# Kernel tuning notes

Measured on AMD Instinct MI355X. Metric: run time of the kernel, lower is better.

The kernel has to match this reference:

```python
import jax, jax.numpy as jnp
import numpy as np
from jax import lax

BOOST_STRENGTH = 0.5
WEIGHT_DENSITY = 0.05


def setup_inputs() -> dict:
    key = jax.random.key(0)
    k1, k2, k3, k4, k5 = jax.random.split(key, 5)
    batch, d_in, d_out = 16384, 512, 4096
    x = jax.random.normal(k1, (batch, d_in), dtype=jnp.float32)
    W = jax.random.normal(k2, (d_out, d_in), dtype=jnp.float32) * 0.05
    b = jax.random.normal(k3, (d_out,), dtype=jnp.float32) * 0.01
    w_mask = (jax.random.uniform(k4, (d_out, d_in)) < WEIGHT_DENSITY).astype(jnp.float32)
    # duty cycle buffer in [0, 0.1]
    duty_cycle = jax.random.uniform(k5, (d_out,), dtype=jnp.float32) * 0.1
    k = 205  # round(0.05 * 4096)
    return {"x": x, "W": W, "b": b, "w_mask": w_mask,
            "duty_cycle": duty_cycle, "k": k}


def reference(x, W, b, w_mask, duty_cycle, k):
    # SparseWeights: masked dense linear
    y = x @ (W * w_mask).T + b                      # [B, n]
    n = y.shape[-1]
    target_density = k / n
    # KWinners boosting: exp of duty-cycle deficit
    boost = jnp.exp(BOOST_STRENGTH * (target_density - duty_cycle))  # [n]
    boosted = y * boost                              # [B, n]
    # top-k threshold per row on boosted values
    thresh = lax.top_k(boosted, k)[0][..., -1:]      # [B, 1]
    # mask: keep ORIGINAL activations at winner positions
    return jnp.where(boosted >= thresh, y, 0.0)
```

## Files before the change

### kernel.cpp

```cpp
#include <hip/hip_runtime.h>
#include <stdint.h>
#include <math.h>


#define BATCH 16384
#define K_DIM 512
#define N_DIM 4096
#define RPB 4
#define MAXE 64

typedef float f32x4 __attribute__((ext_vector_type(4)));
typedef unsigned int u32;

__global__ void boost_kernel(const float* __restrict__ duty,
                             const int* __restrict__ kptr,
                             float* __restrict__ boost) {
  const int j = blockIdx.x * blockDim.x + threadIdx.x;
  if (j < N_DIM) {
    const float td = (float)((double)kptr[0] / (double)N_DIM);
    const float arg = 0.5f * (td - duty[j]);
    boost[j] = (float)exp((double)arg);
  }
}

__global__ __launch_bounds__(256) void compress_kernel(
    const float* __restrict__ W, const float* __restrict__ mask,
    unsigned short* __restrict__ cIdx, float* __restrict__ cVal,
    int* __restrict__ cnt) {
  const int j = blockIdx.x * 4 + (threadIdx.x >> 6);
  const int lane = threadIdx.x & 63;
  if (j >= N_DIM) return;
  const float* mr = mask + (size_t)j * K_DIM;
  const float* wr = W + (size_t)j * K_DIM;
  int base = 0;
#pragma unroll
  for (int c = 0; c < K_DIM / 64; ++c) {
    const int k = c * 64 + lane;
    const bool act = (mr[k] != 0.0f);
    const unsigned long long bal = __ballot(act);
    const int pos = __popcll(bal & ((1ull << lane) - 1ull));
    if (act && base + pos < MAXE) {
      cIdx[(size_t)j * MAXE + base + pos] = (unsigned short)k;
      cVal[(size_t)j * MAXE + base + pos] = wr[k];
    }
    base += (int)__popcll(bal);
  }
  if (lane == 0) cnt[j] = base < MAXE ? base : MAXE;
}

__global__ __launch_bounds__(256) void sort_kernel(
    const int* __restrict__ cnt, int* __restrict__ perm, int* __restrict__ tE) {
  __shared__ int hist[MAXE + 1];
  __shared__ int off[MAXE + 1];
  const int tid = threadIdx.x;
  if (tid <= MAXE) hist[tid] = 0;
  __syncthreads();
  for (int j = tid; j < N_DIM; j += 256) atomicAdd(&hist[cnt[j]], 1);
  __syncthreads();
  if (tid == 0) {
    int s = 0;
    for (int c = 0; c <= MAXE; ++c) { off[c] = s; s += hist[c]; }
  }
  __syncthreads();
  for (int j = tid; j < N_DIM; j += 256) {
    const int p = atomicAdd(&off[cnt[j]], 1);
    perm[p] = j;
  }
  __syncthreads();
  tE[tid] = cnt[perm[tid * 16 + 15]];
}

__global__ __launch_bounds__(256) void fill_kernel(
    const unsigned short* __restrict__ cIdx, const float* __restrict__ cVal,
    const int* __restrict__ cnt, const int* __restrict__ perm,
    uint2* __restrict__ pairT, int* __restrict__ orig) {
  const int s = blockIdx.x * 256 + threadIdx.x;
  const int j = perm[s];
  const int c = cnt[j];
  const int slot = (s & 15) * 256 + (s >> 4);
  orig[slot] = j;
#pragma unroll 4
  for (int e = 0; e < MAXE; ++e) {
    uint2 pr;
    if (e < c) {
      pr.x = (u32)cIdx[(size_t)j * MAXE + e] * 16u;
      pr.y = __float_as_uint(cVal[(size_t)j * MAXE + e]);
    } else {
      pr.x = 0u; pr.y = 0u;
    }
    pairT[(size_t)e * N_DIM + slot] = pr;
  }
}

__global__ __launch_bounds__(256) void fused_kernel(
    const float* __restrict__ x, const float* __restrict__ bvec,
    const uint2* __restrict__ pairT, const float* __restrict__ boost,
    const int* __restrict__ orig, const int* __restrict__ tE,
    const int* __restrict__ kptr, float* __restrict__ out) {
  __shared__ __align__(16) float smem[N_DIM];
  __shared__ u32 hist[256];
  __shared__ u32 s_prefix, s_kk;

  const int tid = threadIdx.x;
  const int row0 = blockIdx.x * RPB;

  for (int i = tid; i < K_DIM; i += 256)
#pragma unroll
    for (int r = 0; r < RPB; ++r)
      smem[i * 4 + r] = x[(size_t)(row0 + r) * K_DIM + i];

  const int myE = tE[tid];
  const int kk0 = kptr[0];
  float a[RPB][16];
#pragma unroll
  for (int r = 0; r < RPB; ++r)
#pragma unroll
    for (int u = 0; u < 16; ++u) a[r][u] = 0.0f;
  __syncthreads();

  for (int e = 0; e < myE; ++e) {
    const uint2* pe = pairT + (size_t)e * N_DIM + tid;
#pragma unroll
    for (int u = 0; u < 16; ++u) {
      const uint2 pr = pe[u * 256];
      const f32x4 xs = *(const f32x4*)((const char*)smem + pr.x);
      const float w = __uint_as_float(pr.y);
      a[0][u] = fmaf(w, xs[0], a[0][u]);
      a[1][u] = fmaf(w, xs[1], a[1][u]);
      a[2][u] = fmaf(w, xs[2], a[2][u]);
      a[3][u] = fmaf(w, xs[3], a[3][u]);
    }
  }

#pragma unroll 1
  for (int r = 0; r < RPB; ++r) {
    __syncthreads();
#pragma unroll
    for (int u = 0; u < 16; ++u)
      smem[orig[u * 256 + tid]] = a[r][u];
    if (tid == 0) { s_prefix = 0u; s_kk = (u32)kk0; }
    __syncthreads();

    float y[16], bl[16];
    u32 key[16];
#pragma unroll
    for (int u = 0; u < 16; ++u) {
      const int j = u * 256 + tid;
      y[u] = smem[j] + bvec[j];
      bl[u] = boost[j];
      const float t = y[u] * bl[u];
      const u32 v = __float_as_uint(t);
      key[u] = (v & 0x80000000u) ? ~v : (v | 0x80000000u);
    }

#pragma unroll 1
    for (int round = 0; round < 4; ++round) {
      const int shift = 24 - 8 * round;
      const u32 prefix = s_prefix;
      const u32 kk = s_kk;
      const u32 himask = round ? (0xFFFFFFFFu << (32 - 8 * round)) : 0u;
      hist[tid] = 0u;
      __syncthreads();
#pragma unroll
      for (int u = 0; u < 16; ++u)
        if ((key[u] & himask) == prefix)
          atomicAdd(&hist[(key[u] >> shift) & 255u], 1u);
      __syncthreads();
      if (tid < 64) {
        const int l = tid;
        const u32 h0 = hist[l * 4], h1 = hist[l * 4 + 1];
        const u32 h2 = hist[l * 4 + 2], h3 = hist[l * 4 + 3];
        const u32 s3 = h3, s2 = h2 + s3, s1 = h1 + s2, s0 = h0 + s1;
        u32 t = s0;
#pragma unroll
        for (int off = 1; off < 64; off <<= 1) {
          const u32 v = __shfl_down(t, off, 64);
          if (l + off < 64) t += v;
        }
        const u32 Eab = t - s0;
        const u32 S[5] = {Eab + s0, Eab + s1, Eab + s2, Eab + s3, Eab};
#pragma unroll
        for (int i = 0; i < 4; ++i)
          if (S[i] >= kk && S[i + 1] < kk) {
            s_prefix = prefix | ((u32)(l * 4 + i) << shift);
            s_kk = kk - S[i + 1];
          }
      }
      __syncthreads();
    }
    const u32 tkey = s_prefix;

    float* orow = out + (size_t)(row0 + r) * N_DIM;
#pragma unroll
    for (int u = 0; u < 16; ++u)
      orow[u * 256 + tid] = (key[u] >= tkey) ? y[u] : 0.0f;
  }
}

extern "C" void kernel_launch(void* const* d_in, const int* in_sizes, int n_in,
                              void* d_out, int out_size, void* d_ws, size_t ws_size,
                              hipStream_t stream) {
  const float* x     = (const float*)d_in[0];
  const float* W     = (const float*)d_in[1];
  const float* bvec  = (const float*)d_in[2];
  const float* wmask = (const float*)d_in[3];
  const float* duty  = (const float*)d_in[4];
  const int* kptr    = (const int*)d_in[5];
  float* out = (float*)d_out;

  uint8_t* ws = (uint8_t*)d_ws;
  unsigned short* cIdx = (unsigned short*)(ws);
  float* cVal          = (float*)(ws + (1u << 20));
  int* cnt             = (int*)(ws + (2u << 20));
  float* boost         = (float*)(ws + (2u << 20) + (64u << 10));
  int* perm            = (int*)(ws + (2u << 20) + (128u << 10));
  int* tE              = (int*)(ws + (2u << 20) + (192u << 10));
  int* orig            = (int*)(ws + (2u << 20) + (256u << 10));
  uint2* pairT         = (uint2*)(ws + (4u << 20));

  boost_kernel<<<16, 256, 0, stream>>>(duty, kptr, boost);
  compress_kernel<<<N_DIM / 4, 256, 0, stream>>>(W, wmask, cIdx, cVal, cnt);
  sort_kernel<<<1, 256, 0, stream>>>(cnt, perm, tE);
  fill_kernel<<<N_DIM / 256, 256, 0, stream>>>(cIdx, cVal, cnt, perm, pairT, orig);
  fused_kernel<<<BATCH / RPB, 256, 0, stream>>>(x, bvec, pairT, boost, orig, tE,
                                                kptr, out);
}
```

Before: 786.5 us.

## Batch radix-select across rows, double-buffer pair loads, raise occupancy hint

The sparse-accumulate loop now double-buffers its index/weight pair loads in registers, so the global loads for the next nonzero overlap with the FMAs on the current one. The per-row radix select is restructured so all four rows are processed together: each wavefront scans one row's histogram in parallel. This cuts the barrier count from about four rounds per row to four rounds in total. Bias and boost are now applied in the permuted domain before the select, and the masked output is scattered through shared memory for coalesced stores. The launch bound of four blocks per CU, together with the extra 32 pair registers, may force register spills.

```diff
diff --git a/kernel.cpp b/kernel.cpp
--- a/kernel.cpp
+++ b/kernel.cpp
@@ -92,14 +92,14 @@
   }
 }
 
-__global__ __launch_bounds__(256) void fused_kernel(
+__global__ __launch_bounds__(256, 4) void fused_kernel(
     const float* __restrict__ x, const float* __restrict__ bvec,
     const uint2* __restrict__ pairT, const float* __restrict__ boost,
     const int* __restrict__ orig, const int* __restrict__ tE,
     const int* __restrict__ kptr, float* __restrict__ out) {
   __shared__ __align__(16) float smem[N_DIM];
-  __shared__ u32 hist[256];
-  __shared__ u32 s_prefix, s_kk;
+  __shared__ u32 hist[4 * 256];
+  __shared__ u32 s_prefix[4], s_kk[4];
 
   const int tid = threadIdx.x;
   const int row0 = blockIdx.x * RPB;
@@ -118,82 +118,127 @@
     for (int u = 0; u < 16; ++u) a[r][u] = 0.0f;
   __syncthreads();
 
-  for (int e = 0; e < myE; ++e) {
-    const uint2* pe = pairT + (size_t)e * N_DIM + tid;
-#pragma unroll
-    for (int u = 0; u < 16; ++u) {
-      const uint2 pr = pe[u * 256];
-      const f32x4 xs = *(const f32x4*)((const char*)smem + pr.x);
-      const float w = __uint_as_float(pr.y);
+  uint2 prA[16], prB[16];
+  {
+    const uint2* p0 = pairT + tid;
+#pragma unroll
+    for (int u = 0; u < 16; ++u) prA[u] = p0[u * 256];
+  }
+  int e = 0;
+  for (; e + 2 <= myE; e += 2) {
+    const uint2* p1 = pairT + (size_t)(e + 1) * N_DIM + tid;
+#pragma unroll
+    for (int u = 0; u < 16; ++u) prB[u] = p1[u * 256];
+#pragma unroll
+    for (int u = 0; u < 16; ++u) {
+      const f32x4 xs = *(const f32x4*)((const char*)smem + prA[u].x);
+      const float w = __uint_as_float(prA[u].y);
       a[0][u] = fmaf(w, xs[0], a[0][u]);
       a[1][u] = fmaf(w, xs[1], a[1][u]);
       a[2][u] = fmaf(w, xs[2], a[2][u]);
       a[3][u] = fmaf(w, xs[3], a[3][u]);
     }
+    const uint2* p2 = pairT + (size_t)(e + 2) * N_DIM + tid;
+#pragma unroll
+    for (int u = 0; u < 16; ++u) prA[u] = p2[u * 256];
+#pragma unroll
+    for (int u = 0; u < 16; ++u) {
+      const f32x4 xs = *(const f32x4*)((const char*)smem + prB[u].x);
+      const float w = __uint_as_float(prB[u].y);
+      a[0][u] = fmaf(w, xs[0], a[0][u]);
+      a[1][u] = fmaf(w, xs[1], a[1][u]);
+      a[2][u] = fmaf(w, xs[2], a[2][u]);
+      a[3][u] = fmaf(w, xs[3], a[3][u]);
+    }
+  }
+  if (e < myE) {
+#pragma unroll
+    for (int u = 0; u < 16; ++u) {
+      const f32x4 xs = *(const f32x4*)((const char*)smem + prA[u].x);
+      const float w = __uint_as_float(prA[u].y);
+      a[0][u] = fmaf(w, xs[0], a[0][u]);
+      a[1][u] = fmaf(w, xs[1], a[1][u]);
+      a[2][u] = fmaf(w, xs[2], a[2][u]);
+      a[3][u] = fmaf(w, xs[3], a[3][u]);
+    }
+  }
+
+  int origId[16];
+  float bl[16];
+#pragma unroll
+  for (int u = 0; u < 16; ++u) origId[u] = orig[u * 256 + tid];
+#pragma unroll
+  for (int u = 0; u < 16; ++u) {
+    const float bj = bvec[origId[u]];
+    bl[u] = boost[origId[u]];
+#pragma unroll
+    for (int r = 0; r < RPB; ++r) a[r][u] += bj;
+  }
+
+  if (tid < 4) { s_prefix[tid] = 0u; s_kk[tid] = (u32)kk0; }
+
+#pragma unroll 1
+  for (int round = 0; round < 4; ++round) {
+    const int shift = 24 - 8 * round;
+    const u32 himask = round ? (0xFFFFFFFFu << (32 - 8 * round)) : 0u;
+#pragma unroll
+    for (int q = 0; q < 4; ++q) hist[q * 256 + tid] = 0u;
+    __syncthreads();
+#pragma unroll
+    for (int r = 0; r < RPB; ++r) {
+      const u32 prefix = s_prefix[r];
+#pragma unroll
+      for (int u = 0; u < 16; ++u) {
+        const float t = a[r][u] * bl[u];
+        const u32 v = __float_as_uint(t);
+        const u32 key = (v & 0x80000000u) ? ~v : (v | 0x80000000u);
+        if ((key & himask) == prefix)
+          atomicAdd(&hist[r * 256 + ((key >> shift) & 255u)], 1u);
+      }
+    }
+    __syncthreads();
+    {
+      const int w = tid >> 6;
+      const int l = tid & 63;
+      const u32 kk = s_kk[w];
+      const u32 prefix = s_prefix[w];
+      const u32 h0 = hist[w * 256 + l * 4],     h1 = hist[w * 256 + l * 4 + 1];
+      const u32 h2 = hist[w * 256 + l * 4 + 2], h3 = hist[w * 256 + l * 4 + 3];
+      const u32 s3 = h3, s2 = h2 + s3, s1 = h1 + s2, s0 = h0 + s1;
+      u32 t = s0;
+#pragma unroll
+      for (int off = 1; off < 64; off <<= 1) {
+        const u32 v = __shfl_down(t, off, 64);
+        if (l + off < 64) t += v;
+      }
+      const u32 Eab = t - s0;
+      const u32 S[5] = {Eab + s0, Eab + s1, Eab + s2, Eab + s3, Eab};
+#pragma unroll
+      for (int i = 0; i < 4; ++i)
+        if (S[i] >= kk && S[i + 1] < kk) {
+          s_prefix[w] = prefix | ((u32)(l * 4 + i) << shift);
+          s_kk[w] = kk - S[i + 1];
+        }
+    }
+    __syncthreads();
   }
 
 #pragma unroll 1
   for (int r = 0; r < RPB; ++r) {
-    __syncthreads();
+    const u32 tkey = s_prefix[r];
+    __syncthreads();
+#pragma unroll
+    for (int u = 0; u < 16; ++u) {
+      const float t = a[r][u] * bl[u];
+      const u32 v = __float_as_uint(t);
+      const u32 key = (v & 0x80000000u) ? ~v : (v | 0x80000000u);
+      smem[origId[u]] = (key >= tkey) ? a[r][u] : 0.0f;
+    }
+    __syncthreads();
+    float* orow = out + (size_t)(row0 + r) * N_DIM;
 #pragma unroll
     for (int u = 0; u < 16; ++u)
-      smem[orig[u * 256 + tid]] = a[r][u];
-    if (tid == 0) { s_prefix = 0u; s_kk = (u32)kk0; }
-    __syncthreads();
-
-    float y[16], bl[16];
-    u32 key[16];
-#pragma unroll
-    for (int u = 0; u < 16; ++u) {
-      const int j = u * 256 + tid;
-      y[u] = smem[j] + bvec[j];
-      bl[u] = boost[j];
-      const float t = y[u] * bl[u];
-      const u32 v = __float_as_uint(t);
-      key[u] = (v & 0x80000000u) ? ~v : (v | 0x80000000u);
-    }
-
-#pragma unroll 1
-    for (int round = 0; round < 4; ++round) {
-      const int shift = 24 - 8 * round;
-      const u32 prefix = s_prefix;
-      const u32 kk = s_kk;
-      const u32 himask = round ? (0xFFFFFFFFu << (32 - 8 * round)) : 0u;
-      hist[tid] = 0u;
-      __syncthreads();
-#pragma unroll
-      for (int u = 0; u < 16; ++u)
-        if ((key[u] & himask) == prefix)
-          atomicAdd(&hist[(key[u] >> shift) & 255u], 1u);
-      __syncthreads();
-      if (tid < 64) {
-        const int l = tid;
-        const u32 h0 = hist[l * 4], h1 = hist[l * 4 + 1];
-        const u32 h2 = hist[l * 4 + 2], h3 = hist[l * 4 + 3];
-        const u32 s3 = h3, s2 = h2 + s3, s1 = h1 + s2, s0 = h0 + s1;
-        u32 t = s0;
-#pragma unroll
-        for (int off = 1; off < 64; off <<= 1) {
-          const u32 v = __shfl_down(t, off, 64);
-          if (l + off < 64) t += v;
-        }
-        const u32 Eab = t - s0;
-        const u32 S[5] = {Eab + s0, Eab + s1, Eab + s2, Eab + s3, Eab};
-#pragma unroll
-        for (int i = 0; i < 4; ++i)
-          if (S[i] >= kk && S[i + 1] < kk) {
-            s_prefix = prefix | ((u32)(l * 4 + i) << shift);
-            s_kk = kk - S[i + 1];
-          }
-      }
-      __syncthreads();
-    }
-    const u32 tkey = s_prefix;
-
-    float* orow = out + (size_t)(row0 + r) * N_DIM;
-#pragma unroll
-    for (int u = 0; u < 16; ++u)
-      orow[u * 256 + tid] = (key[u] >= tkey) ? y[u] : 0.0f;
+      orow[u * 256 + tid] = smem[u * 256 + tid];
   }
 }
 
```

Result: slower. 1.297 ms (+64.8%).

## Radix-select on fixed-point keys in permuted order, add tie-break pass

Applied to the files above, without the earlier changes.

Adds the bias and boost gathers in the permuted column order up front, so the per-row scatter to shared memory before selection goes away. The radix select now runs on keys rebuilt each round from a fixed-point integer conversion of the boosted value instead of stored float-bit keys, which frees the key registers. A small tie-resolution pass compares exact float keys inside the final fixed-point bucket, capped at 16 candidates, to recover the exact threshold. Results are scattered through shared memory so the global stores stay coalesced. This costs extra arithmetic per round and an extra barrier and serial step, and the tie cap plus fixed-point clamping could be wrong in rare cases.

```diff
diff --git a/kernel.cpp b/kernel.cpp
--- a/kernel.cpp
+++ b/kernel.cpp
@@ -8,6 +8,7 @@
 #define N_DIM 4096
 #define RPB 4
 #define MAXE 64
+#define TCAP 16
 
 typedef float f32x4 __attribute__((ext_vector_type(4)));
 typedef unsigned int u32;
@@ -92,14 +93,26 @@
   }
 }
 
-__global__ __launch_bounds__(256) void fused_kernel(
+static __device__ __forceinline__ u32 ikey(float t) {
+  float s = t * 268435456.0f;
+  s = fminf(fmaxf(s, -2.1e9f), 2.1e9f);
+  return ((u32)(int)s) ^ 0x80000000u;
+}
+static __device__ __forceinline__ u32 fkey(float t) {
+  const u32 v = __float_as_uint(t);
+  return (v & 0x80000000u) ? ~v : (v | 0x80000000u);
+}
+
+__global__ void fused_kernel(
     const float* __restrict__ x, const float* __restrict__ bvec,
     const uint2* __restrict__ pairT, const float* __restrict__ boost,
     const int* __restrict__ orig, const int* __restrict__ tE,
     const int* __restrict__ kptr, float* __restrict__ out) {
   __shared__ __align__(16) float smem[N_DIM];
   __shared__ u32 hist[256];
-  __shared__ u32 s_prefix, s_kk;
+  __shared__ u32 s_prefix, s_kk, s_cut;
+  __shared__ int s_tc;
+  __shared__ u32 s_tie[TCAP];
 
   const int tid = threadIdx.x;
   const int row0 = blockIdx.x * RPB;
@@ -132,43 +145,39 @@
     }
   }
 
+  float bl[16];
+#pragma unroll
+  for (int u = 0; u < 16; ++u) {
+    const int j = orig[u * 256 + tid];
+    const float bj = bvec[j];
+    bl[u] = boost[j];
+#pragma unroll
+    for (int r = 0; r < RPB; ++r) a[r][u] += bj;
+  }
+
 #pragma unroll 1
   for (int r = 0; r < RPB; ++r) {
     __syncthreads();
-#pragma unroll
-    for (int u = 0; u < 16; ++u)
-      smem[orig[u * 256 + tid]] = a[r][u];
-    if (tid == 0) { s_prefix = 0u; s_kk = (u32)kk0; }
-    __syncthreads();
-
-    float y[16], bl[16];
-    u32 key[16];
-#pragma unroll
-    for (int u = 0; u < 16; ++u) {
-      const int j = u * 256 + tid;
-      y[u] = smem[j] + bvec[j];
-      bl[u] = boost[j];
-      const float t = y[u] * bl[u];
-      const u32 v = __float_as_uint(t);
-      key[u] = (v & 0x80000000u) ? ~v : (v | 0x80000000u);
-    }
+    if (tid == 0) { s_prefix = 0u; s_kk = (u32)kk0; s_tc = 0; s_cut = 0u; }
 
 #pragma unroll 1
     for (int round = 0; round < 4; ++round) {
       const int shift = 24 - 8 * round;
-      const u32 prefix = s_prefix;
-      const u32 kk = s_kk;
       const u32 himask = round ? (0xFFFFFFFFu << (32 - 8 * round)) : 0u;
       hist[tid] = 0u;
       __syncthreads();
-#pragma unroll
-      for (int u = 0; u < 16; ++u)
-        if ((key[u] & himask) == prefix)
-          atomicAdd(&hist[(key[u] >> shift) & 255u], 1u);
+      const u32 prefix = s_prefix;
+      const u32 kk = s_kk;
+#pragma unroll
+      for (int u = 0; u < 16; ++u) {
+        const u32 U = ikey(a[r][u] * bl[u]);
+        if ((U & himask) == prefix)
+          atomicAdd(&hist[(U >> shift) & 255u], 1u);
+      }
       __syncthreads();
       if (tid < 64) {
         const int l = tid;
-        const u32 h0 = hist[l * 4], h1 = hist[l * 4 + 1];
+        const u32 h0 = hist[l * 4],     h1 = hist[l * 4 + 1];
         const u32 h2 = hist[l * 4 + 2], h3 = hist[l * 4 + 3];
         const u32 s3 = h3, s2 = h2 + s3, s1 = h1 + s2, s0 = h0 + s1;
         u32 t = s0;
@@ -188,12 +197,47 @@
       }
       __syncthreads();
     }
-    const u32 tkey = s_prefix;
-
+    const u32 Uk = s_prefix;
+#pragma unroll
+    for (int u = 0; u < 16; ++u) {
+      const float t = a[r][u] * bl[u];
+      if (ikey(t) == Uk) {
+        const int idx = atomicAdd(&s_tc, 1);
+        if (idx < TCAP) s_tie[idx] = fkey(t);
+      }
+    }
+    __syncthreads();
+    if (tid == 0) {
+      const int C = s_tc < TCAP ? s_tc : TCAP;
+      const int m = (int)s_kk;
+      u32 cut = 0u;
+      if (m < C) {
+        u32 vals[TCAP];
+        for (int i = 0; i < C; ++i) vals[i] = s_tie[i];
+        for (int t2 = 0; t2 < m; ++t2) {
+          int best = 0; u32 bv = 0u;
+          for (int i = 0; i < C; ++i)
+            if (vals[i] >= bv) { bv = vals[i]; best = i; }
+          cut = bv; vals[best] = 0u;
+        }
+      }
+      s_cut = cut;
+    }
+    __syncthreads();
+    const u32 cut = s_cut;
+
+#pragma unroll
+    for (int u = 0; u < 16; ++u) {
+      const float t = a[r][u] * bl[u];
+      const u32 U = ikey(t);
+      const bool win = (U > Uk) || (U == Uk && fkey(t) >= cut);
+      smem[orig[u * 256 + tid]] = win ? a[r][u] : 0.0f;
+    }
+    __syncthreads();
     float* orow = out + (size_t)(row0 + r) * N_DIM;
 #pragma unroll
     for (int u = 0; u < 16; ++u)
-      orow[u * 256 + tid] = (key[u] >= tkey) ? y[u] : 0.0f;
+      orow[u * 256 + tid] = smem[u * 256 + tid];
   }
 }
 
```

After: 1.159 ms. +47.4%, slower.
